# Kernel optimization log

Hardware: AMD Instinct MI355X
Metric: run time of the kernel (lower is better)

Reference implementation:

```python
import jax, jax.numpy as jnp
import numpy as np
import math

B, S, E, H = 2, 1024, 1024, 8
HD = E // H
M, W, K, GH, R, MR = 128, 32, 8, 128, 8, 8
ATTN_ALPHA, GATE_TEMP, CONTENT_MIX = 3.0, 1.0, 0.25
FFN_H = 4 * E


def _layernorm(z, g, b):
    mu = jnp.mean(z, axis=-1, keepdims=True)
    var = jnp.var(z, axis=-1, keepdims=True)
    return (z - mu) * jax.lax.rsqrt(var + 1e-5) * g + b


def _topk_sparse(logits, k, temp):
    # faithful to torch topk_sparse_weights: hard + (soft - hard).detach()
    soft = jax.nn.softmax(logits / max(temp, 1e-6), axis=-1)
    idx = jax.lax.top_k(soft, k)[1]
    hard = jax.nn.one_hot(idx, logits.shape[-1], dtype=soft.dtype).sum(axis=-2)
    hard = hard / (hard.sum(axis=-1, keepdims=True) + 1e-8)
    return hard + jax.lax.stop_gradient(soft - hard)


def _pos_and_window():
    rel = jnp.arange(-(S - 1), S, dtype=jnp.float32)  # [2S-1]
    p1 = rel / S
    p2 = jnp.sign(rel) * jnp.sqrt(jnp.abs(rel) + 1e-6) / math.sqrt(S)
    pos_kern = jnp.stack([p1, p2], axis=-1)  # [2S-1, 2]
    d = jnp.arange(S, dtype=jnp.float32)
    sigma = S / 4.0
    win = jnp.exp(-(d ** 2) / (2.0 * sigma ** 2))  # [S]
    return pos_kern, win


def setup_inputs() -> dict:
    key = jax.random.key(0)
    ks = jax.random.split(key, 20)
    rn = lambda i, shape, s: jax.random.normal(ks[i], shape, dtype=jnp.float32) * s
    scale = 1.0 / math.sqrt(HD)
    return {
        'x': rn(0, (B, S, E), 1.0),
        'v_w': rn(1, (E, E), 0.02), 'v_b': jnp.zeros((E,), jnp.float32),
        'out_w': rn(2, (E, E), 0.02), 'out_b': jnp.zeros((E,), jnp.float32),
        'qmod_w': rn(3, (E, H), 0.02), 'qmod_b': jnp.zeros((H,), jnp.float32),
        'kmod_w': rn(4, (E, H), 0.02), 'kmod_b': jnp.zeros((H,), jnp.float32),
        'gate_w1': rn(5, (H, E, GH), 0.02), 'gate_b1': jnp.zeros((H, GH), jnp.float32),
        'gate_w2': rn(6, (H, GH, M), 0.02), 'gate_b2': jnp.zeros((H, M), jnp.float32),
        'mod_w1': rn(7, (H, E, GH), 0.02), 'mod_b1': jnp.zeros((H, GH), jnp.float32),
        'mod_w2': rn(8, (H, GH, MR), 0.02), 'mod_b2': jnp.zeros((H, MR), jnp.float32),
        'mod_basis': rn(9, (H, MR, M), 0.05),
        'freqs': rn(10, (H, M, W, 2), 1.5),
        'amps': rn(11, (H, M, W), 0.02) + 0.5,
        'phases': rn(12, (H, M, W), math.pi),
        'content_wq': rn(13, (H, HD, R), scale),
        'content_wk': rn(14, (H, HD, R), scale),
        'ffn_w1': rn(15, (E, FFN_H), 0.02), 'ffn_b1': jnp.zeros((FFN_H,), jnp.float32),
        'ffn_w2': rn(16, (FFN_H, E), 0.02), 'ffn_b2': jnp.zeros((E,), jnp.float32),
        'ln_attn_g': jnp.ones((E,), jnp.float32), 'ln_attn_b': jnp.zeros((E,), jnp.float32),
        'ln_ffn_g': jnp.ones((E,), jnp.float32), 'ln_ffn_b': jnp.zeros((E,), jnp.float32),
    }


def reference(x, v_w, v_b, out_w, out_b, qmod_w, qmod_b, kmod_w, kmod_b,
              gate_w1, gate_b1, gate_w2, gate_b2, mod_w1, mod_b1, mod_w2, mod_b2,
              mod_basis, freqs, amps, phases, content_wq, content_wk,
              ffn_w1, ffn_b1, ffn_w2, ffn_b2, ln_attn_g, ln_attn_b, ln_ffn_g, ln_ffn_b):
    pos_kern, win = _pos_and_window()
    # --- per-sequence gating over mask library (top-k sparse routing) ---
    pooled = x.mean(axis=1)  # [B,E]
    gh = jax.nn.relu(jnp.einsum('be,heg->bhg', pooled, gate_w1) + gate_b1)
    glog = jnp.einsum('bhg,hgm->bhm', gh, gate_w2) + gate_b2  # [B,H,M]
    wsel = _topk_sparse(glog, K, GATE_TEMP)
    mh = jax.nn.relu(jnp.einsum('be,heg->bhg', pooled, mod_w1) + mod_b1)
    mr = jnp.einsum('bhg,hgr->bhr', mh, mod_w2) + mod_b2  # [B,H,MR]
    mod = jnp.einsum('bhr,hrm->bhm', mr, mod_basis)
    wmod = wsel * (1.0 + mod)  # [B,H,M]
    # --- wave-interference synthesis of relative-position kernels ---
    dots = jnp.einsum('ld,hmwd->hmwl', pos_kern, freqs)  # [H,M,W,2S-1]
    waves = jnp.sin(2.0 * math.pi * dots + phases[..., None]) * amps[..., None]
    kernels = waves.sum(axis=2)  # [H,M,2S-1]
    kern = jnp.einsum('bhm,hml->bhl', wmod, kernels)  # [B,H,2S-1]
    # --- Toeplitz gather into causal score matrix ---
    i = jnp.arange(S)
    rel_idx = (i[None, :] - i[:, None]) + (S - 1)  # index of rel = j - i
    scores = kern[:, :, rel_idx]  # [B,H,S,S]
    dist = jnp.clip(i[:, None] - i[None, :], 0, S - 1)
    scores = scores * win[dist]
    qs = x @ qmod_w + qmod_b  # [B,S,H]
    km = x @ kmod_w + kmod_b
    logits = ATTN_ALPHA * scores + qs.transpose(0, 2, 1)[..., None] + km.transpose(0, 2, 1)[:, :, None, :]
    # --- low-rank content term ---
    xh = x.reshape(B, S, H, HD)
    qc = jnp.einsum('bshd,hdr->bhsr', xh, content_wq)
    kc = jnp.einsum('bshd,hdr->bhsr', xh, content_wk)
    logits = logits + CONTENT_MIX * jnp.einsum('bhsr,bhtr->bhst', qc, kc)
    causal = i[:, None] >= i[None, :]
    logits = jnp.where(causal, logits, -jnp.inf)
    attn = jax.nn.softmax(logits, axis=-1)
    v = (x @ v_w + v_b).reshape(B, S, H, HD)
    o = jnp.einsum('bhst,bthd->bshd', attn, v).reshape(B, S, E)
    o = o @ out_w + out_b
    y = _layernorm(x + o, ln_attn_g, ln_attn_b)
    f = jax.nn.gelu(y @ ffn_w1 + ffn_b1) @ ffn_w2 + ffn_b2
    return _layernorm(y + f, ln_ffn_g, ln_ffn_b)
```

## Files before the change

kernel.cpp:

```cpp
#include <hip/hip_runtime.h>
#include <math.h>
#include <stdint.h>

namespace {

constexpr int B_ = 2, S_ = 1024, E_ = 1024, H_ = 8, HD_ = 128;
constexpr int M_ = 128, W_ = 32, GH_ = 128, R_ = 8, MR_ = 8, FFNH_ = 4096;
constexpr int SCH = 32;
constexpr int SPC = S_ / SCH;

typedef __bf16 bf16;
typedef _Float16 f16;
typedef __attribute__((ext_vector_type(8))) __bf16 bf16x8;
typedef __attribute__((ext_vector_type(4))) __bf16 bf16x4;
typedef __attribute__((ext_vector_type(4))) _Float16 f16x4;
typedef __attribute__((ext_vector_type(4))) float f32x4;

__device__ inline float gelu_tanh(float u) {
  float u3 = u * u * u;
  return 0.5f * u * (1.f + tanhf(0.7978845608028654f * (u + 0.044715f * u3)));
}

__device__ __forceinline__ void gl_lds16(const void* g, void* l) {
  __builtin_amdgcn_global_load_lds((const __attribute__((address_space(1))) void*)g,
                                   (__attribute__((address_space(3))) void*)l, 16, 0, 0);
}

__global__ __launch_bounds__(256) void k_prep(
    const float* __restrict__ x, bf16* __restrict__ xb,
    const float* __restrict__ v_w, bf16* __restrict__ vwT,
    const float* __restrict__ out_w, bf16* __restrict__ outwT,
    const float* __restrict__ ffn_w1, bf16* __restrict__ ffn1T,
    const float* __restrict__ ffn_w2, bf16* __restrict__ ffn2T,
    const float* __restrict__ qmw, const float* __restrict__ kmw,
    const float* __restrict__ cwq, const float* __restrict__ cwk,
    bf16* __restrict__ wcat, float* __restrict__ part,
    const float* __restrict__ freqs, const float* __restrict__ amps,
    const float* __restrict__ phases, float* __restrict__ kerns) {
  __shared__ float tile[32][33];
  __shared__ float f0[W_], f1[W_], am[W_], ph[W_];
  int b = blockIdx.x, t = threadIdx.x;
  if (b < 2048) {
    size_t i = ((size_t)b * 256 + t) * 4;
    float4 v = *(const float4*)(x + i);
    bf16x4 o;
    o.x = (bf16)v.x; o.y = (bf16)v.y; o.z = (bf16)v.z; o.w = (bf16)v.w;
    *(bf16x4*)(xb + i) = o;
    return;
  }
  if (b < 12288) {
    const float* w; bf16* wT; int K, N, bx, by;
    if (b < 3072) {
      w = v_w; wT = vwT; K = 1024; N = 1024;
      int l = b - 2048; bx = l & 31; by = l >> 5;
    } else if (b < 4096) {
      w = out_w; wT = outwT; K = 1024; N = 1024;
      int l = b - 3072; bx = l & 31; by = l >> 5;
    } else if (b < 8192) {
      w = ffn_w1; wT = ffn1T; K = 1024; N = 4096;
      int l = b - 4096; bx = l & 127; by = l >> 7;
    } else {
      w = ffn_w2; wT = ffn2T; K = 4096; N = 1024;
      int l = b - 8192; bx = l & 31; by = l >> 5;
    }
    int n0 = bx * 32, k0 = by * 32;
    int tx = t & 31, ty = t >> 5;
    for (int r = ty; r < 32; r += 8) tile[r][tx] = w[(size_t)(k0 + r) * N + n0 + tx];
    __syncthreads();
    for (int r = ty; r < 32; r += 8) wT[(size_t)(n0 + r) * K + k0 + tx] = (bf16)tile[tx][r];
    return;
  }
  if (b < 13312) {
    int idx = (b - 12288) * 256 + t;
    int n = idx >> 10, k = idx & 1023;
    float v = 0.f;
    if (n < 8) {
      v = qmw[k * 8 + n];
    } else if (n < 16) {
      v = kmw[k * 8 + (n - 8)];
    } else if (n < 80) {
      int u = n - 16, h = u >> 3, r = u & 7;
      int kk = k - h * 128;
      if (kk >= 0 && kk < 128) v = cwq[((size_t)h * 128 + kk) * 8 + r];
    } else if (n < 144) {
      int u = n - 80, h = u >> 3, r = u & 7;
      int kk = k - h * 128;
      if (kk >= 0 && kk < 128) v = cwk[((size_t)h * 128 + kk) * 8 + r];
    }
    wcat[idx] = (bf16)v;
    return;
  }
  if (b < 13376) {
    int b0 = b - 13312;
    int bb = b0 / SCH, c = b0 % SCH;
    const float* xp = x + (size_t)bb * S_ * E_ + (size_t)c * SPC * E_;
    float acc[4] = {0.f, 0.f, 0.f, 0.f};
    for (int s = 0; s < SPC; ++s) {
      const float* row = xp + (size_t)s * E_;
#pragma unroll
      for (int q = 0; q < 4; ++q) acc[q] += row[t + q * 256];
    }
    float* pp = part + (size_t)b0 * E_;
#pragma unroll
    for (int q = 0; q < 4; ++q) pp[t + q * 256] = acc[q];
    return;
  }
  {
    int blk = b - 13376;
    int lt = blk & 3;
    int hm = blk >> 2;
    if (t < W_) {
      f0[t] = freqs[((size_t)hm * W_ + t) * 2 + 0];
      f1[t] = freqs[((size_t)hm * W_ + t) * 2 + 1];
      am[t] = amps[(size_t)hm * W_ + t];
      ph[t] = phases[(size_t)hm * W_ + t];
    }
    __syncthreads();
    int l = lt * 256 + t;
    float rel = (float)(l - (S_ - 1));
    float p1 = rel * (1.0f / S_);
    float p2 = (rel < 0.f) ? (-sqrtf(-rel + 1e-6f) * (1.0f / 32.0f)) : 0.f;
    const float TWO_PI = 6.28318530717958647692f;
    float acc = 0.f;
#pragma unroll
    for (int w = 0; w < W_; ++w)
      acc += am[w] * __sinf(TWO_PI * (f0[w] * p1 + f1[w] * p2) + ph[w]);
    kerns[(size_t)hm * S_ + l] = acc;
  }
}

__global__ __launch_bounds__(256) void k_fin_qk(
    const f16* __restrict__ P, const float* __restrict__ qmb,
    const float* __restrict__ kmb, float* __restrict__ qsT,
    float* __restrict__ kmT, float* __restrict__ qc, float* __restrict__ kc) {
  int row = blockIdx.x;
  int t = threadIdx.x;
  if (t >= 144) return;
  int b = row >> 10, s = row & 1023;
  const size_t mn = (size_t)2048 * 256;
  float sum = 0.f;
#pragma unroll
  for (int z = 0; z < 8; ++z) sum += (float)P[(size_t)z * mn + (size_t)row * 256 + t];
  if (t < 8) {
    qsT[((size_t)(b * 8 + t)) * 1024 + s] = sum + qmb[t];
  } else if (t < 16) {
    kmT[((size_t)(b * 8 + t - 8)) * 1024 + s] = sum + kmb[t - 8];
  } else if (t < 80) {
    int u = t - 16, h = u >> 3, r = u & 7;
    qc[(((size_t)(b * 8 + h)) * 1024 + s) * 8 + r] = sum;
  } else {
    int u = t - 80, h = u >> 3, r = u & 7;
    kc[(((size_t)(b * 8 + h)) * 1024 + s) * 8 + r] = sum;
  }
}

__global__ __launch_bounds__(256) void k_gate1(
    const float* __restrict__ part,
    const float* __restrict__ gw1, const float* __restrict__ mw1,
    float2* __restrict__ outp) {
  int chunk = blockIdx.x;
  int h = blockIdx.y;
  int mat = blockIdx.z;
  const float* w = mat ? mw1 : gw1;
  int t = threadIdx.x;
  __shared__ float spool[2][64];
  if (t < 128) {
    int bb = t >> 6;
    int e = chunk * 64 + (t & 63);
    float s = 0.f;
    for (int c = 0; c < SCH; ++c) s += part[(size_t)(bb * SCH + c) * E_ + e];
    spool[bb][t & 63] = s * (1.0f / S_);
  }
  __syncthreads();
  int g = t & 127, half = t >> 7;
  int e0 = chunk * 64 + half * 32;
  const float* wp = w + (size_t)h * E_ * GH_ + (size_t)e0 * GH_ + g;
  float a0 = 0.f, a1 = 0.f;
#pragma unroll 8
  for (int r = 0; r < 32; ++r) {
    float wv = wp[(size_t)r * GH_];
    a0 += spool[0][half * 32 + r] * wv;
    a1 += spool[1][half * 32 + r] * wv;
  }
  __shared__ float red[2][2][128];
  red[half][0][g] = a0;
  red[half][1][g] = a1;
  __syncthreads();
  if (half == 0) {
    float2 o;
    o.x = red[0][0][g] + red[1][0][g];
    o.y = red[0][1][g] + red[1][1][g];
    outp[(((size_t)mat * H_ + h) * 16 + chunk) * 128 + g] = o;
  }
}

__global__ __launch_bounds__(256) void k_gate2(
    const float2* __restrict__ part,
    const float* __restrict__ gb1, const float* __restrict__ gw2, const float* __restrict__ gb2,
    const float* __restrict__ mb1, const float* __restrict__ mw2, const float* __restrict__ mb2,
    const float* __restrict__ mbasis, float* __restrict__ wmod) {
  int bh = blockIdx.x;
  int b = bh >> 3, h = bh & 7;
  int t = threadIdx.x;
  __shared__ float ghs[GH_], mhs[GH_], glog[M_], mrs[MR_];
  __shared__ float red2[2][128];
  __shared__ float rbuf[128];
  {
    int g = t & 127, mat = t >> 7;
    const float2* pp = part + ((size_t)mat * H_ + h) * 16 * 128 + g;
    float acc = 0.f;
#pragma unroll
    for (int c = 0; c < 16; ++c) {
      float2 v = pp[(size_t)c * 128];
      acc += b ? v.y : v.x;
    }
    acc += (mat ? mb1 : gb1)[h * GH_ + g];
    acc = fmaxf(acc, 0.f);
    if (mat == 0) ghs[g] = acc; else mhs[g] = acc;
  }
  __syncthreads();
  {
    int m = t & 127, half = t >> 7;
    float acc = 0.f;
    const float* wp = gw2 + (size_t)h * GH_ * M_ + m;
#pragma unroll 4
    for (int g = half * 64; g < half * 64 + 64; ++g)
      acc += ghs[g] * wp[(size_t)g * M_];
    red2[half][m] = acc;
  }
  __syncthreads();
  if (t < 128) glog[t] = red2[0][t] + red2[1][t] + gb2[h * M_ + t];
  if (t < 64) {
    int r = t & 7, seg = t >> 3;
    float acc = 0.f;
    const float* wp = mw2 + (size_t)h * GH_ * MR_ + r;
    for (int g = seg * 16; g < seg * 16 + 16; ++g) acc += mhs[g] * wp[(size_t)g * MR_];
    acc += __shfl_xor(acc, 8);
    acc += __shfl_xor(acc, 16);
    acc += __shfl_xor(acc, 32);
    if (t < 8) mrs[t] = acc + mb2[h * MR_ + t];
  }
  __syncthreads();
  if (t < 128) rbuf[t] = glog[t];
  __syncthreads();
  for (int off = 64; off >= 1; off >>= 1) {
    if (t < off) rbuf[t] = fmaxf(rbuf[t], rbuf[t + off]);
    __syncthreads();
  }
  float mx = rbuf[0];
  __syncthreads();
  float ev = 0.f;
  if (t < 128) ev = expf(glog[t] - mx);
  __syncthreads();
  if (t < 128) rbuf[t] = ev;
  __syncthreads();
  for (int off = 64; off >= 1; off >>= 1) {
    if (t < off) rbuf[t] += rbuf[t + off];
    __syncthreads();
  }
  float inv = 1.f / rbuf[0];
  if (t < 128) {
    float wsel = ev * inv;
    float md = 0.f;
#pragma unroll
    for (int r = 0; r < MR_; ++r) md += mrs[r] * mbasis[((size_t)h * MR_ + r) * M_ + t];
    wmod[bh * M_ + t] = wsel * (1.f + md);
  }
}

__global__ __launch_bounds__(256) void k_cont(const float* __restrict__ qc,
                                              const float* __restrict__ kc,
                                              bf16* __restrict__ cont,
                                              const float* __restrict__ wmod,
                                              const float* __restrict__ kerns,
                                              float* __restrict__ swin) {
  int jt = blockIdx.x, it = blockIdx.y;
  int bh = blockIdx.z;
  int t = threadIdx.x;
  if (bh == 16) {
    __shared__ float wm[M_];
    int blk = it * 8 + jt;
    int dt = blk & 3;
    int sbh = blk >> 2;
    int h = sbh & 7;
    if (t < M_) wm[t] = wmod[sbh * M_ + t];
    __syncthreads();
    int d = dt * 256 + t;
    int l = (S_ - 1) - d;
    float acc = 0.f;
    for (int m = 0; m < M_; ++m) acc += wm[m] * kerns[((size_t)h * M_ + m) * S_ + l];
    float dd = (float)d;
    float win = expf(-dd * dd * (1.0f / 131072.0f));
    swin[(size_t)sbh * S_ + d] = 3.0f * win * acc;
    return;
  }
  if (jt > it) return;
  int w = t >> 6, lane = t & 63;
  int ln = lane & 15, ko = lane >> 4;
  int i0 = it * 128 + w * 32;
  int j0 = jt * 128;

  bf16x8 av[2];
#pragma unroll
  for (int mi = 0; mi < 2; ++mi) {
    bf16x8 a;
#pragma unroll
    for (int k = 0; k < 8; ++k) a[k] = (bf16)0.f;
    if (ko == 0) {
      const float* qp = &qc[((size_t)bh * S_ + i0 + mi * 16 + ln) * 8];
      float4 q0 = *(const float4*)qp;
      float4 q1 = *(const float4*)(qp + 4);
      a[0] = (bf16)q0.x; a[1] = (bf16)q0.y; a[2] = (bf16)q0.z; a[3] = (bf16)q0.w;
      a[4] = (bf16)q1.x; a[5] = (bf16)q1.y; a[6] = (bf16)q1.z; a[7] = (bf16)q1.w;
    }
    av[mi] = a;
  }
  bf16x8 bv[8];
#pragma unroll
  for (int nb = 0; nb < 8; ++nb) {
    bf16x8 bb;
#pragma unroll
    for (int k = 0; k < 8; ++k) bb[k] = (bf16)0.f;
    if (ko == 0) {
      const float* kp = &kc[((size_t)bh * S_ + j0 + nb * 16 + ln) * 8];
      float4 k0 = *(const float4*)kp;
      float4 k1 = *(const float4*)(kp + 4);
      bb[0] = (bf16)k0.x; bb[1] = (bf16)k0.y; bb[2] = (bf16)k0.z; bb[3] = (bf16)k0.w;
      bb[4] = (bf16)k1.x; bb[5] = (bf16)k1.y; bb[6] = (bf16)k1.z; bb[7] = (bf16)k1.w;
    }
    bv[nb] = bb;
  }
  f32x4 acc[2][8];
#pragma unroll
  for (int mi = 0; mi < 2; ++mi)
#pragma unroll
    for (int nb = 0; nb < 8; ++nb) {
      acc[mi][nb] = (f32x4){0.f, 0.f, 0.f, 0.f};
      acc[mi][nb] = __builtin_amdgcn_mfma_f32_16x16x32_bf16(av[mi], bv[nb], acc[mi][nb], 0, 0, 0);
    }
  bf16* cb = cont + ((size_t)bh << 20);
#pragma unroll
  for (int mi = 0; mi < 2; ++mi)
#pragma unroll
    for (int nb = 0; nb < 8; ++nb) {
      int col = j0 + nb * 16 + ln;
#pragma unroll
      for (int reg = 0; reg < 4; ++reg) {
        int row = i0 + mi * 16 + ko * 4 + reg;
        cb[(size_t)row * S_ + col] = (bf16)acc[mi][nb][reg];
      }
    }
}

template <bool GELU, bool RES, bool OUTF32, bool OUTBF16>
__global__ __launch_bounds__(256) void k_gemm_mfma(
    const bf16* __restrict__ A, const bf16* __restrict__ BT,
    const float* __restrict__ bias, const float* __restrict__ res,
    float* __restrict__ C, bf16* __restrict__ Cb, int N, int K) {
  __shared__ bf16 Asb[2][8192];
  __shared__ bf16 Bsb[2][8192];
  int t = threadIdx.x;
  int gx = gridDim.x, gy = gridDim.y;
  int nwg = gx * gy;
  int lin = blockIdx.y * gx + blockIdx.x;
  if (!(nwg & 7)) {
    int cpx = nwg >> 3;
    lin = (lin & 7) * cpx + (lin >> 3);
  }
  int by = lin % gy;
  int bx = lin / gy;
  int row0 = by * 128, col0 = bx * 128;
  int lane = t & 63, wid = t >> 6;
  int wr = wid >> 1, wc = wid & 1;

  const bf16* AgP[4];
  const bf16* BgP[4];
  int ldo[4];
#pragma unroll
  for (int j = 0; j < 4; ++j) {
    int p = t + j * 256;
    int sub = p >> 9;
    int pp = p & 511;
    int rt = ((pp >> 6) << 4) | (pp & 15);
    int kb = (pp >> 4) & 3;
    AgP[j] = A + (size_t)(row0 + rt) * K + sub * 32 + kb * 8;
    BgP[j] = BT + (size_t)(col0 + rt) * K + sub * 32 + kb * 8;
    ldo[j] = sub * 4096 + pp * 8;
  }

  f32x4 acc[4][4];
#pragma unroll
  for (int m = 0; m < 4; ++m)
#pragma unroll
    for (int n = 0; n < 4; ++n) acc[m][n] = (f32x4){0.f, 0.f, 0.f, 0.f};

#pragma unroll
  for (int j = 0; j < 4; ++j) {
    gl_lds16(AgP[j], &Asb[0][ldo[j]]);
    gl_lds16(BgP[j], &Bsb[0][ldo[j]]);
  }

  const int nt = K >> 6;
  for (int kt = 0; kt < nt; ++kt) {
    int cur = kt & 1;
    __syncthreads();
    if (kt + 1 < nt) {
      size_t go = (size_t)(kt + 1) * 64;
      int nb = cur ^ 1;
#pragma unroll
      for (int j = 0; j < 4; ++j) {
        gl_lds16(AgP[j] + go, &Asb[nb][ldo[j]]);
        gl_lds16(BgP[j] + go, &Bsb[nb][ldo[j]]);
      }
    }
#pragma unroll
    for (int kk = 0; kk < 2; ++kk) {
      bf16x8 af[4], bfr[4];
#pragma unroll
      for (int m = 0; m < 4; ++m)
        af[m] = *(const bf16x8*)&Asb[cur][kk * 4096 + ((wr * 4 + m) * 64 + lane) * 8];
#pragma unroll
      for (int n = 0; n < 4; ++n)
        bfr[n] = *(const bf16x8*)&Bsb[cur][kk * 4096 + ((wc * 4 + n) * 64 + lane) * 8];
#pragma unroll
      for (int m = 0; m < 4; ++m)
#pragma unroll
        for (int n = 0; n < 4; ++n)
          acc[m][n] = __builtin_amdgcn_mfma_f32_16x16x32_bf16(af[m], bfr[n], acc[m][n], 0, 0, 0);
    }
  }

  int r0 = row0 + wr * 64, c0 = col0 + wc * 64;
#pragma unroll
  for (int m = 0; m < 4; ++m) {
#pragma unroll
    for (int n = 0; n < 4; ++n) {
      int col = c0 + n * 16 + (lane & 15);
      float bcol = bias[col];
#pragma unroll
      for (int reg = 0; reg < 4; ++reg) {
        int row = r0 + m * 16 + ((lane >> 4) << 2) + reg;
        float u = acc[m][n][reg] + bcol;
        if (GELU) u = gelu_tanh(u);
        if (RES) u += res[(size_t)row * N + col];
        if (OUTF32) C[(size_t)row * N + col] = u;
        if (OUTBF16) Cb[(size_t)row * N + col] = (bf16)u;
      }
    }
  }
}

template <int NB>
__global__ __launch_bounds__(256) void k_gemm_sk(
    const bf16* __restrict__ A, const bf16* __restrict__ BT,
    f16* __restrict__ P, int N, int K, int Kslice, size_t strideB, size_t mn) {
  __shared__ bf16 Asb[2][8192];
  __shared__ bf16 Bsb[2][8192];
  int t = threadIdx.x;
  int gx = gridDim.x, gy = gridDim.y;
  int nwg = gx * gy * gridDim.z;
  int lin = (blockIdx.z * gy + blockIdx.y) * gx + blockIdx.x;
  if (!(nwg & 7)) {
    int cpx = nwg >> 3;
    lin = (lin & 7) * cpx + (lin >> 3);
  }
  int by = lin % gy;
  int rem = lin / gy;
  int bx = rem % gx;
  int z = rem / gx;

  int bb = z % NB;
  int k0 = (z / NB) * Kslice;
  const bf16* Bbase = BT + (size_t)bb * strideB;
  int row0 = by * 128, col0 = bx * 128;
  int lane = t & 63, wid = t >> 6;
  int wr = wid >> 1, wc = wid & 1;

  const bf16* AgP[4];
  const bf16* BgP[4];
  int ldo[4];
#pragma unroll
  for (int j = 0; j < 4; ++j) {
    int p = t + j * 256;
    int sub = p >> 9;
    int pp = p & 511;
    int rt = ((pp >> 6) << 4) | (pp & 15);
    int kb = (pp >> 4) & 3;
    AgP[j] = A + (size_t)(row0 + rt) * K + k0 + sub * 32 + kb * 8;
    BgP[j] = Bbase + (size_t)(col0 + rt) * K + k0 + sub * 32 + kb * 8;
    ldo[j] = sub * 4096 + pp * 8;
  }

  f32x4 acc[4][4];
#pragma unroll
  for (int m = 0; m < 4; ++m)
#pragma unroll
    for (int n = 0; n < 4; ++n) acc[m][n] = (f32x4){0.f, 0.f, 0.f, 0.f};

#pragma unroll
  for (int j = 0; j < 4; ++j) {
    gl_lds16(AgP[j], &Asb[0][ldo[j]]);
    gl_lds16(BgP[j], &Bsb[0][ldo[j]]);
  }

  const int nt = Kslice >> 6;
  for (int kt = 0; kt < nt; ++kt) {
    int cur = kt & 1;
    __syncthreads();
    if (kt + 1 < nt) {
      size_t go = (size_t)(kt + 1) * 64;
      int nb = cur ^ 1;
#pragma unroll
      for (int j = 0; j < 4; ++j) {
        gl_lds16(AgP[j] + go, &Asb[nb][ldo[j]]);
        gl_lds16(BgP[j] + go, &Bsb[nb][ldo[j]]);
      }
    }
#pragma unroll
    for (int kk = 0; kk < 2; ++kk) {
      bf16x8 af[4], bfr[4];
#pragma unroll
      for (int m = 0; m < 4; ++m)
        af[m] = *(const bf16x8*)&Asb[cur][kk * 4096 + ((wr * 4 + m) * 64 + lane) * 8];
#pragma unroll
      for (int n = 0; n < 4; ++n)
        bfr[n] = *(const bf16x8*)&Bsb[cur][kk * 4096 + ((wc * 4 + n) * 64 + lane) * 8];
#pragma unroll
      for (int m = 0; m < 4; ++m)
#pragma unroll
        for (int n = 0; n < 4; ++n)
          acc[m][n] = __builtin_amdgcn_mfma_f32_16x16x32_bf16(af[m], bfr[n], acc[m][n], 0, 0, 0);
    }
  }

  f16* Pz = P + (size_t)z * mn;
  int r0 = row0 + wr * 64, c0 = col0 + wc * 64;
#pragma unroll
  for (int m = 0; m < 4; ++m)
#pragma unroll
    for (int n = 0; n < 4; ++n) {
      int col = c0 + n * 16 + (lane & 15);
#pragma unroll
      for (int reg = 0; reg < 4; ++reg) {
        int row = r0 + m * 16 + ((lane >> 4) << 2) + reg;
        Pz[(size_t)row * N + col] = (f16)acc[m][n][reg];
      }
    }
}

__global__ __launch_bounds__(256) void k_fin_vT(const f16* __restrict__ P,
                                                const float* __restrict__ bias,
                                                bf16* __restrict__ vT) {
  size_t i = ((size_t)blockIdx.x * 256 + threadIdx.x) * 4;
  const size_t mn = (size_t)1024 * 1024;
  float sx = 0.f, sy = 0.f, sz = 0.f, sw2 = 0.f;
#pragma unroll
  for (int sk = 0; sk < 4; ++sk) {
    f16x4 v = *(const f16x4*)&P[(size_t)sk * 2 * mn + i];
    sx += (float)v.x; sy += (float)v.y; sz += (float)v.z; sw2 += (float)v.w;
  }
  float bcol = bias[(i >> 10) & 1023];
  bf16x4 o;
  o.x = (bf16)(sx + bcol); o.y = (bf16)(sy + bcol);
  o.z = (bf16)(sz + bcol); o.w = (bf16)(sw2 + bcol);
  *(bf16x4*)&vT[i] = o;
}

template <int SK, bool OUTBF16>
__global__ __launch_bounds__(256) void k_fin_ln(
    const f16* __restrict__ P, const float* __restrict__ bias,
    const float* __restrict__ res, const float* __restrict__ g,
    const float* __restrict__ bb, float* __restrict__ outF,
    bf16* __restrict__ outB) {
  int row = blockIdx.x, t = threadIdx.x;
  size_t base = (size_t)row * E_ + t * 4;
  const size_t mn = (size_t)2048 * 1024;
  float u0 = 0.f, u1 = 0.f, u2 = 0.f, u3 = 0.f;
#pragma unroll
  for (int sk = 0; sk < SK; ++sk) {
    f16x4 v = *(const f16x4*)&P[(size_t)sk * mn + base];
    u0 += (float)v.x; u1 += (float)v.y; u2 += (float)v.z; u3 += (float)v.w;
  }
  float4 bv = *(const float4*)&bias[t * 4];
  float4 rv = *(const float4*)&res[base];
  u0 += bv.x + rv.x; u1 += bv.y + rv.y; u2 += bv.z + rv.z; u3 += bv.w + rv.w;
  float s = u0 + u1 + u2 + u3;
  float s2 = u0 * u0 + u1 * u1 + u2 * u2 + u3 * u3;
#pragma unroll
  for (int off = 32; off >= 1; off >>= 1) {
    s += __shfl_xor(s, off);
    s2 += __shfl_xor(s2, off);
  }
  __shared__ float rs[4], rs2[4];
  int wid = t >> 6;
  if ((t & 63) == 0) { rs[wid] = s; rs2[wid] = s2; }
  __syncthreads();
  float S1 = rs[0] + rs[1] + rs[2] + rs[3];
  float S2 = rs2[0] + rs2[1] + rs2[2] + rs2[3];
  float mu = S1 * (1.f / E_);
  float var = S2 * (1.f / E_) - mu * mu;
  float inv = rsqrtf(var + 1e-5f);
  float4 gv = *(const float4*)&g[t * 4];
  float4 bbv = *(const float4*)&bb[t * 4];
  float4 ov;
  ov.x = (u0 - mu) * inv * gv.x + bbv.x;
  ov.y = (u1 - mu) * inv * gv.y + bbv.y;
  ov.z = (u2 - mu) * inv * gv.z + bbv.z;
  ov.w = (u3 - mu) * inv * gv.w + bbv.w;
  *(float4*)&outF[base] = ov;
  if (OUTBF16) {
    bf16x4 obv;
    obv.x = (bf16)ov.x; obv.y = (bf16)ov.y; obv.z = (bf16)ov.z; obv.w = (bf16)ov.w;
    *(bf16x4*)&outB[base] = obv;
  }
}

__global__ __launch_bounds__(256) void k_attn2(
    const float* __restrict__ qsT, const float* __restrict__ kmT,
    const bf16* __restrict__ cont, const float* __restrict__ swin,
    const bf16* __restrict__ vT,
    bf16* __restrict__ o, bf16* __restrict__ opart, float* __restrict__ mlpart) {
  int q = blockIdx.x & 3;
  int iwg = blockIdx.x >> 2;
  if (q > iwg) return;
  int bh = blockIdx.y;
  int b = bh >> 3, h = bh & 7;
  int t = threadIdx.x;
  int wid = t >> 6, lane = t & 63;
  int iw = iwg * 4 + wid;
  int m = lane & 15, ko = lane >> 4;
  int ntile = iwg + 1;

  __shared__ float sw[S_];
  *(float4*)&sw[t * 4] = *(const float4*)&swin[(size_t)bh * S_ + t * 4];
  __syncthreads();

  int i_row = iw * 16 + m;
  float qs_i = qsT[(size_t)bh * S_ + i_row];
  const bf16* cr = cont + ((size_t)bh << 20) + (size_t)i_row * S_;

  f32x4 acc[8];
#pragma unroll
  for (int nf = 0; nf < 8; ++nf) acc[nf] = (f32x4){0.f, 0.f, 0.f, 0.f};
  float m_run = -INFINITY, l_run = 0.f;

  for (int jt = q; jt < ntile; jt += 4) {
    int j0 = jt * 64;
    float pv[2][8];
    float mx = -INFINITY;
    bf16x8 cv[2];
    cv[0] = *(const bf16x8*)&cr[j0 + ko * 8];
    cv[1] = *(const bf16x8*)&cr[j0 + 32 + ko * 8];
#pragma unroll
    for (int s = 0; s < 2; ++s) {
      int bj = j0 + s * 32 + ko * 8;
      float4 km0 = *(const float4*)&kmT[(size_t)bh * S_ + bj];
      float4 km1 = *(const float4*)&kmT[(size_t)bh * S_ + bj + 4];
      float kmv[8] = {km0.x, km0.y, km0.z, km0.w, km1.x, km1.y, km1.z, km1.w};
#pragma unroll
      for (int e = 0; e < 8; ++e) {
        int j = bj + e;
        int dd = i_row - j;
        float val = sw[dd >= 0 ? dd : 0] + qs_i + kmv[e] + 0.25f * (float)cv[s][e];
        val = (dd >= 0) ? val : -INFINITY;
        pv[s][e] = val;
        mx = fmaxf(mx, val);
      }
    }
    mx = fmaxf(mx, __shfl_xor(mx, 16));
    mx = fmaxf(mx, __shfl_xor(mx, 32));
    float mnew = fmaxf(m_run, mx);
    float scale = __expf(m_run - mnew);
    float lsum = 0.f;
    bf16x8 pa[2];
#pragma unroll
    for (int s = 0; s < 2; ++s)
#pragma unroll
      for (int e = 0; e < 8; ++e) {
        float p = __expf(pv[s][e] - mnew);
        lsum += p;
        pa[s][e] = (bf16)p;
      }
    lsum += __shfl_xor(lsum, 16);
    lsum += __shfl_xor(lsum, 32);
    l_run = l_run * scale + lsum;
    m_run = mnew;
    float sc[4];
#pragma unroll
    for (int r = 0; r < 4; ++r) sc[r] = __shfl(scale, ko * 4 + r);
#pragma unroll
    for (int nf = 0; nf < 8; ++nf)
#pragma unroll
      for (int r = 0; r < 4; ++r) acc[nf][r] *= sc[r];
#pragma unroll
    for (int s = 0; s < 2; ++s) {
      int bj = j0 + s * 32 + ko * 8;
#pragma unroll
      for (int nf = 0; nf < 8; ++nf) {
        int d = nf * 16 + m;
        bf16x8 bv = *(const bf16x8*)&vT[((size_t)bh * HD_ + d) * S_ + bj];
        acc[nf] = __builtin_amdgcn_mfma_f32_16x16x32_bf16(pa[s], bv, acc[nf], 0, 0, 0);
      }
    }
  }

  if (ntile == 1) {
    float lr[4];
#pragma unroll
    for (int r = 0; r < 4; ++r) lr[r] = __shfl(l_run, ko * 4 + r);
#pragma unroll
    for (int nf = 0; nf < 8; ++nf) {
      int d = nf * 16 + m;
#pragma unroll
      for (int r = 0; r < 4; ++r) {
        int row = iw * 16 + ko * 4 + r;
        o[(((size_t)b * S_ + row) * H_ + h) * HD_ + d] = (bf16)(acc[nf][r] / lr[r]);
      }
    }
  } else {
    bf16* op = opart + ((size_t)(q * 16 + bh) * 64 + iw) * 2048;
#pragma unroll
    for (int nf = 0; nf < 8; ++nf) {
      int d = nf * 16 + m;
#pragma unroll
      for (int r = 0; r < 4; ++r) op[(ko * 4 + r) * 128 + d] = (bf16)acc[nf][r];
    }
    if (lane < 16) {
      float* mlp = mlpart + ((size_t)(q * 16 + bh) * 64 + iw) * 32;
      mlp[m * 2 + 0] = m_run;
      mlp[m * 2 + 1] = l_run;
    }
  }
}

__global__ __launch_bounds__(256) void k_comb(const bf16* __restrict__ opart,
                                              const float* __restrict__ mlpart,
                                              bf16* __restrict__ o) {
  int blk = blockIdx.x;
  int bh = blk / 60, iw = blk % 60 + 4;
  int b = bh >> 3, h = bh & 7;
  int t = threadIdx.x;
  int r = t >> 4, d0 = (t & 15) * 8;
  int nq = iw / 4 + 1;
  if (nq > 4) nq = 4;
  float mq[4], lq[4];
  float mm = -INFINITY;
#pragma unroll
  for (int q = 0; q < 4; ++q) {
    if (q < nq) {
      size_t idx = (size_t)(q * 16 + bh) * 64 + iw;
      mq[q] = mlpart[idx * 32 + r * 2];
      lq[q] = mlpart[idx * 32 + r * 2 + 1];
      mm = fmaxf(mm, mq[q]);
    }
  }
  float L = 0.f;
  float acc[8] = {0.f, 0.f, 0.f, 0.f, 0.f, 0.f, 0.f, 0.f};
#pragma unroll
  for (int q = 0; q < 4; ++q) {
    if (q < nq) {
      float e = __expf(mq[q] - mm);
      L += lq[q] * e;
      size_t idx = (size_t)(q * 16 + bh) * 64 + iw;
      bf16x8 v = *(const bf16x8*)&opart[(idx * 16 + r) * 128 + d0];
#pragma unroll
      for (int k = 0; k < 8; ++k) acc[k] += (float)v[k] * e;
    }
  }
  float inv = 1.f / L;
  bf16x8 ov;
#pragma unroll
  for (int k = 0; k < 8; ++k) ov[k] = (bf16)(acc[k] * inv);
  int row = iw * 16 + r;
  *(bf16x8*)&o[(((size_t)b * S_ + row) * H_ + h) * HD_ + d0] = ov;
}

}

extern "C" void kernel_launch(void* const* d_in, const int* in_sizes, int n_in,
                              void* d_out, int out_size, void* d_ws, size_t ws_size,
                              hipStream_t stream) {
  (void)in_sizes; (void)n_in; (void)out_size; (void)ws_size;
  const float* x       = (const float*)d_in[0];
  const float* v_w     = (const float*)d_in[1];
  const float* v_b     = (const float*)d_in[2];
  const float* out_w   = (const float*)d_in[3];
  const float* out_b   = (const float*)d_in[4];
  const float* qmod_w  = (const float*)d_in[5];
  const float* qmod_b  = (const float*)d_in[6];
  const float* kmod_w  = (const float*)d_in[7];
  const float* kmod_b  = (const float*)d_in[8];
  const float* gate_w1 = (const float*)d_in[9];
  const float* gate_b1 = (const float*)d_in[10];
  const float* gate_w2 = (const float*)d_in[11];
  const float* gate_b2 = (const float*)d_in[12];
  const float* mod_w1  = (const float*)d_in[13];
  const float* mod_b1  = (const float*)d_in[14];
  const float* mod_w2  = (const float*)d_in[15];
  const float* mod_b2  = (const float*)d_in[16];
  const float* mod_basis = (const float*)d_in[17];
  const float* freqs   = (const float*)d_in[18];
  const float* amps    = (const float*)d_in[19];
  const float* phases  = (const float*)d_in[20];
  const float* cwq     = (const float*)d_in[21];
  const float* cwk     = (const float*)d_in[22];
  const float* ffn_w1  = (const float*)d_in[23];
  const float* ffn_b1  = (const float*)d_in[24];
  const float* ffn_w2  = (const float*)d_in[25];
  const float* ffn_b2  = (const float*)d_in[26];
  const float* ln_ag   = (const float*)d_in[27];
  const float* ln_ab   = (const float*)d_in[28];
  const float* ln_fg   = (const float*)d_in[29];
  const float* ln_fb   = (const float*)d_in[30];

  char* wsc = (char*)d_ws;
  size_t off = 0;
  auto alloc = [&](size_t bytes) -> void* {
    void* p = wsc + off;
    off += (bytes + 255) & ~(size_t)255;
    return p;
  };
  float* pooled = (float*)alloc(2048 * 4);
  float* part   = (float*)alloc(65536 * 4);
  float2* gpart = (float2*)alloc((size_t)2 * H_ * 16 * 128 * 8);
  float* wmod   = (float*)alloc(2048 * 4);
  float* kerns  = (float*)alloc((size_t)H_ * M_ * S_ * 4);
  float* swin   = (float*)alloc((size_t)B_ * H_ * S_ * 4);
  float* qsT    = (float*)alloc((size_t)B_ * H_ * S_ * 4);
  float* kmT    = (float*)alloc((size_t)B_ * H_ * S_ * 4);
  float* qcb    = (float*)alloc((size_t)B_ * H_ * S_ * R_ * 4);
  float* kcb    = (float*)alloc((size_t)B_ * H_ * S_ * R_ * 4);
  float* ybuf   = (float*)alloc((size_t)B_ * S_ * E_ * 4);
  bf16* xb      = (bf16*)alloc((size_t)B_ * S_ * E_ * 2);
  bf16* yb      = (bf16*)alloc((size_t)B_ * S_ * E_ * 2);
  bf16* vwT     = (bf16*)alloc((size_t)E_ * E_ * 2);
  bf16* outwT   = (bf16*)alloc((size_t)E_ * E_ * 2);
  bf16* ffn1T   = (bf16*)alloc((size_t)E_ * FFNH_ * 2);
  bf16* ffn2T   = (bf16*)alloc((size_t)FFNH_ * E_ * 2);
  bf16* wcatT   = (bf16*)alloc((size_t)256 * E_ * 2);
  bf16* vT      = (bf16*)alloc((size_t)B_ * S_ * E_ * 2);
  bf16* ob      = (bf16*)alloc((size_t)B_ * S_ * E_ * 2);
  float* mlpart = (float*)alloc((size_t)4 * 16 * 64 * 16 * 2 * 4);
  char* poolU2  = (char*)alloc((size_t)B_ * S_ * FFNH_ * 2);
  bf16* opart = (bf16*)poolU2;
  bf16* hb    = (bf16*)poolU2;
  char* P1c = (char*)alloc((size_t)64 * 1024 * 1024);
  f16*  P1  = (f16*)P1c;
  bf16* cont = (bf16*)(P1c + (size_t)16 * 1024 * 1024);
  (void)pooled;

  float* outp = (float*)d_out;
  const int BS = B_ * S_;

  k_prep<<<17472, 256, 0, stream>>>(x, xb, v_w, vwT, out_w, outwT,
                                    ffn_w1, ffn1T, ffn_w2, ffn2T,
                                    qmod_w, kmod_w, cwq, cwk, wcatT,
                                    part, freqs, amps, phases, kerns);

  k_gate1<<<dim3(16, H_, 2), 256, 0, stream>>>(part, gate_w1, mod_w1, gpart);
  k_gate2<<<B_ * H_, 256, 0, stream>>>(gpart, gate_b1, gate_w2, gate_b2,
                                       mod_b1, mod_w2, mod_b2, mod_basis, wmod);

  k_gemm_sk<1><<<dim3(2, 16, 8), 256, 0, stream>>>(
      xb, wcatT, P1, 256, E_, 128, 0, (size_t)2048 * 256);
  k_fin_qk<<<2048, 256, 0, stream>>>(P1, qmod_b, kmod_b, qsT, kmT, qcb, kcb);

  k_cont<<<dim3(8, 8, 17), 256, 0, stream>>>(qcb, kcb, cont, wmod, kerns, swin);

  k_gemm_sk<2><<<dim3(8, 8, 8), 256, 0, stream>>>(
      vwT, xb, P1, S_, E_, 256, (size_t)S_ * E_, (size_t)1024 * 1024);
  k_fin_vT<<<2048, 256, 0, stream>>>(P1, v_b, vT);

  k_attn2<<<dim3(64, 16), 256, 0, stream>>>(qsT, kmT, cont, swin, vT, ob, opart, mlpart);
  k_comb<<<16 * 60, 256, 0, stream>>>(opart, mlpart, ob);

  k_gemm_sk<1><<<dim3(8, 16, 4), 256, 0, stream>>>(
      ob, outwT, P1, E_, E_, 256, 0, (size_t)2048 * 1024);
  k_fin_ln<4, true><<<2048, 256, 0, stream>>>(P1, out_b, x, ln_ag, ln_ab, ybuf, yb);

  k_gemm_mfma<true, false, false, true><<<dim3(FFNH_ / 128, BS / 128), 256, 0, stream>>>(
      yb, ffn1T, ffn_b1, nullptr, nullptr, hb, FFNH_, E_);

  k_gemm_sk<1><<<dim3(8, 16, 4), 256, 0, stream>>>(
      hb, ffn2T, P1, E_, FFNH_, 1024, 0, (size_t)2048 * 1024);
  k_fin_ln<4, false><<<2048, 256, 0, stream>>>(P1, ffn_b2, ybuf, ln_fg, ln_fb, outp, nullptr);
}
```

Baseline: 236.5 us.

## Merge independent pre-attention kernels into shared launches by block-index partitioning

The GEMM mainloop moves into a reusable device function. Three pairs of independent kernels now share one launch each, with the work picked by block index: the q/k projection GEMM with the first gate layer, the q/k finalization with the second gate layer, and the content/window kernel with the value projection GEMM. This cuts the number of kernel launches and the gaps between them, and lets unrelated small workloads run alongside the GEMMs. In exchange, every block in a merged launch reserves the GEMM's larger LDS footprint, which can lower occupancy for the lightweight branches.

```diff
diff --git a/kernel.cpp b/kernel.cpp
--- a/kernel.cpp
+++ b/kernel.cpp
@@ -24,6 +24,95 @@
 __device__ __forceinline__ void gl_lds16(const void* g, void* l) {
   __builtin_amdgcn_global_load_lds((const __attribute__((address_space(1))) void*)g,
                                    (__attribute__((address_space(3))) void*)l, 16, 0, 0);
+}
+
+template <int NB>
+__device__ __forceinline__ void gemm_body(
+    const bf16* __restrict__ A, const bf16* __restrict__ BT,
+    f16* __restrict__ P, int N, int K, int Kslice, size_t strideB, size_t mn,
+    int lin, int gx, int gy, bf16* Asb, bf16* Bsb) {
+  int t = threadIdx.x;
+  int by = lin % gy;
+  int rem = lin / gy;
+  int bx = rem % gx;
+  int z = rem / gx;
+  int bb = z % NB;
+  int k0 = (z / NB) * Kslice;
+  const bf16* Bbase = BT + (size_t)bb * strideB;
+  int row0 = by * 128, col0 = bx * 128;
+  int lane = t & 63, wid = t >> 6;
+  int wr = wid >> 1, wc = wid & 1;
+
+  const bf16* AgP[4];
+  const bf16* BgP[4];
+  int ldo[4];
+#pragma unroll
+  for (int j = 0; j < 4; ++j) {
+    int p = t + j * 256;
+    int sub = p >> 9;
+    int pp = p & 511;
+    int rt = ((pp >> 6) << 4) | (pp & 15);
+    int kb = (pp >> 4) & 3;
+    AgP[j] = A + (size_t)(row0 + rt) * K + k0 + sub * 32 + kb * 8;
+    BgP[j] = Bbase + (size_t)(col0 + rt) * K + k0 + sub * 32 + kb * 8;
+    ldo[j] = sub * 4096 + pp * 8;
+  }
+
+  f32x4 acc[4][4];
+#pragma unroll
+  for (int m = 0; m < 4; ++m)
+#pragma unroll
+    for (int n = 0; n < 4; ++n) acc[m][n] = (f32x4){0.f, 0.f, 0.f, 0.f};
+
+#pragma unroll
+  for (int j = 0; j < 4; ++j) {
+    gl_lds16(AgP[j], &Asb[ldo[j]]);
+    gl_lds16(BgP[j], &Bsb[ldo[j]]);
+  }
+
+  const int nt = Kslice >> 6;
+  for (int kt = 0; kt < nt; ++kt) {
+    int cur = kt & 1;
+    __syncthreads();
+    if (kt + 1 < nt) {
+      size_t go = (size_t)(kt + 1) * 64;
+      int nb = cur ^ 1;
+#pragma unroll
+      for (int j = 0; j < 4; ++j) {
+        gl_lds16(AgP[j] + go, &Asb[nb * 8192 + ldo[j]]);
+        gl_lds16(BgP[j] + go, &Bsb[nb * 8192 + ldo[j]]);
+      }
+    }
+#pragma unroll
+    for (int kk = 0; kk < 2; ++kk) {
+      bf16x8 af[4], bfr[4];
+#pragma unroll
+      for (int m = 0; m < 4; ++m)
+        af[m] = *(const bf16x8*)&Asb[cur * 8192 + kk * 4096 + ((wr * 4 + m) * 64 + lane) * 8];
+#pragma unroll
+      for (int n = 0; n < 4; ++n)
+        bfr[n] = *(const bf16x8*)&Bsb[cur * 8192 + kk * 4096 + ((wc * 4 + n) * 64 + lane) * 8];
+#pragma unroll
+      for (int m = 0; m < 4; ++m)
+#pragma unroll
+        for (int n = 0; n < 4; ++n)
+          acc[m][n] = __builtin_amdgcn_mfma_f32_16x16x32_bf16(af[m], bfr[n], acc[m][n], 0, 0, 0);
+    }
+  }
+
+  f16* Pz = P + (size_t)z * mn;
+  int r0 = row0 + wr * 64, c0 = col0 + wc * 64;
+#pragma unroll
+  for (int m = 0; m < 4; ++m)
+#pragma unroll
+    for (int n = 0; n < 4; ++n) {
+      int col = c0 + n * 16 + (lane & 15);
+#pragma unroll
+      for (int reg = 0; reg < 4; ++reg) {
+        int row = r0 + m * 16 + ((lane >> 4) << 2) + reg;
+        Pz[(size_t)row * N + col] = (f16)acc[m][n][reg];
+      }
+    }
 }
 
 __global__ __launch_bounds__(256) void k_prep(
@@ -129,41 +218,26 @@
   }
 }
 
-__global__ __launch_bounds__(256) void k_fin_qk(
-    const f16* __restrict__ P, const float* __restrict__ qmb,
-    const float* __restrict__ kmb, float* __restrict__ qsT,
-    float* __restrict__ kmT, float* __restrict__ qc, float* __restrict__ kc) {
-  int row = blockIdx.x;
-  int t = threadIdx.x;
-  if (t >= 144) return;
-  int b = row >> 10, s = row & 1023;
-  const size_t mn = (size_t)2048 * 256;
-  float sum = 0.f;
-#pragma unroll
-  for (int z = 0; z < 8; ++z) sum += (float)P[(size_t)z * mn + (size_t)row * 256 + t];
-  if (t < 8) {
-    qsT[((size_t)(b * 8 + t)) * 1024 + s] = sum + qmb[t];
-  } else if (t < 16) {
-    kmT[((size_t)(b * 8 + t - 8)) * 1024 + s] = sum + kmb[t - 8];
-  } else if (t < 80) {
-    int u = t - 16, h = u >> 3, r = u & 7;
-    qc[(((size_t)(b * 8 + h)) * 1024 + s) * 8 + r] = sum;
-  } else {
-    int u = t - 80, h = u >> 3, r = u & 7;
-    kc[(((size_t)(b * 8 + h)) * 1024 + s) * 8 + r] = sum;
-  }
-}
-
-__global__ __launch_bounds__(256) void k_gate1(
+__global__ __launch_bounds__(256) void k_qkg(
+    const bf16* __restrict__ xb, const bf16* __restrict__ wcatT,
+    f16* __restrict__ P,
     const float* __restrict__ part,
     const float* __restrict__ gw1, const float* __restrict__ mw1,
-    float2* __restrict__ outp) {
-  int chunk = blockIdx.x;
-  int h = blockIdx.y;
-  int mat = blockIdx.z;
+    float2* __restrict__ gpart) {
+  __shared__ bf16 Asb[2 * 8192];
+  __shared__ bf16 Bsb[2 * 8192];
+  __shared__ float spool[2][64];
+  __shared__ float red[2][2][128];
+  int b = blockIdx.x, t = threadIdx.x;
+  if (b < 256) {
+    int lin = (b & 7) * 32 + (b >> 3);
+    gemm_body<1>(xb, wcatT, P, 256, E_, 128, 0, (size_t)2048 * 256,
+                 lin, 2, 16, Asb, Bsb);
+    return;
+  }
+  int b0 = b - 256;
+  int chunk = b0 & 15, h = (b0 >> 4) & 7, mat = b0 >> 7;
   const float* w = mat ? mw1 : gw1;
-  int t = threadIdx.x;
-  __shared__ float spool[2][64];
   if (t < 128) {
     int bb = t >> 6;
     int e = chunk * 64 + (t & 63);
@@ -182,7 +256,6 @@
     a0 += spool[0][half * 32 + r] * wv;
     a1 += spool[1][half * 32 + r] * wv;
   }
-  __shared__ float red[2][2][128];
   red[half][0][g] = a0;
   red[half][1][g] = a1;
   __syncthreads();
@@ -190,24 +263,48 @@
     float2 o;
     o.x = red[0][0][g] + red[1][0][g];
     o.y = red[0][1][g] + red[1][1][g];
-    outp[(((size_t)mat * H_ + h) * 16 + chunk) * 128 + g] = o;
-  }
-}
-
-__global__ __launch_bounds__(256) void k_gate2(
-    const float2* __restrict__ part,
+    gpart[(((size_t)mat * H_ + h) * 16 + chunk) * 128 + g] = o;
+  }
+}
+
+__global__ __launch_bounds__(256) void k_fg2(
+    const f16* __restrict__ P, const float* __restrict__ qmb,
+    const float* __restrict__ kmb, float* __restrict__ qsT,
+    float* __restrict__ kmT, float* __restrict__ qc, float* __restrict__ kc,
+    const float2* __restrict__ gpart,
     const float* __restrict__ gb1, const float* __restrict__ gw2, const float* __restrict__ gb2,
     const float* __restrict__ mb1, const float* __restrict__ mw2, const float* __restrict__ mb2,
     const float* __restrict__ mbasis, float* __restrict__ wmod) {
-  int bh = blockIdx.x;
-  int b = bh >> 3, h = bh & 7;
-  int t = threadIdx.x;
   __shared__ float ghs[GH_], mhs[GH_], glog[M_], mrs[MR_];
   __shared__ float red2[2][128];
   __shared__ float rbuf[128];
+  int blk = blockIdx.x, t = threadIdx.x;
+  if (blk < 2048) {
+    if (t >= 144) return;
+    int row = blk;
+    int b = row >> 10, s = row & 1023;
+    const size_t mn = (size_t)2048 * 256;
+    float sum = 0.f;
+#pragma unroll
+    for (int z = 0; z < 8; ++z) sum += (float)P[(size_t)z * mn + (size_t)row * 256 + t];
+    if (t < 8) {
+      qsT[((size_t)(b * 8 + t)) * 1024 + s] = sum + qmb[t];
+    } else if (t < 16) {
+      kmT[((size_t)(b * 8 + t - 8)) * 1024 + s] = sum + kmb[t - 8];
+    } else if (t < 80) {
+      int u = t - 16, h = u >> 3, r = u & 7;
+      qc[(((size_t)(b * 8 + h)) * 1024 + s) * 8 + r] = sum;
+    } else {
+      int u = t - 80, h = u >> 3, r = u & 7;
+      kc[(((size_t)(b * 8 + h)) * 1024 + s) * 8 + r] = sum;
+    }
+    return;
+  }
+  int bh = blk - 2048;
+  int b = bh >> 3, h = bh & 7;
   {
     int g = t & 127, mat = t >> 7;
-    const float2* pp = part + ((size_t)mat * H_ + h) * 16 * 128 + g;
+    const float2* pp = gpart + ((size_t)mat * H_ + h) * 16 * 128 + g;
     float acc = 0.f;
 #pragma unroll
     for (int c = 0; c < 16; ++c) {
@@ -268,17 +365,26 @@
   }
 }
 
-__global__ __launch_bounds__(256) void k_cont(const float* __restrict__ qc,
-                                              const float* __restrict__ kc,
-                                              bf16* __restrict__ cont,
-                                              const float* __restrict__ wmod,
-                                              const float* __restrict__ kerns,
-                                              float* __restrict__ swin) {
-  int jt = blockIdx.x, it = blockIdx.y;
-  int bh = blockIdx.z;
-  int t = threadIdx.x;
+__global__ __launch_bounds__(256) void k_cv(
+    const float* __restrict__ qc, const float* __restrict__ kc,
+    bf16* __restrict__ cont,
+    const float* __restrict__ wmod, const float* __restrict__ kerns,
+    float* __restrict__ swin,
+    const bf16* __restrict__ vwT, const bf16* __restrict__ xb,
+    f16* __restrict__ P) {
+  __shared__ bf16 Asb[2 * 8192];
+  __shared__ bf16 Bsb[2 * 8192];
+  __shared__ float wm[M_];
+  int b = blockIdx.x, t = threadIdx.x;
+  if (b >= 1088) {
+    int l = b - 1088;
+    int lin = (l & 7) * 64 + (l >> 3);
+    gemm_body<2>(vwT, xb, P, S_, E_, 256, (size_t)S_ * E_, (size_t)1024 * 1024,
+                 lin, 8, 8, Asb, Bsb);
+    return;
+  }
+  int jt = b & 7, it = (b >> 3) & 7, bh = b >> 6;
   if (bh == 16) {
-    __shared__ float wm[M_];
     int blk = it * 8 + jt;
     int dt = blk & 3;
     int sbh = blk >> 2;
@@ -454,9 +560,8 @@
 __global__ __launch_bounds__(256) void k_gemm_sk(
     const bf16* __restrict__ A, const bf16* __restrict__ BT,
     f16* __restrict__ P, int N, int K, int Kslice, size_t strideB, size_t mn) {
-  __shared__ bf16 Asb[2][8192];
-  __shared__ bf16 Bsb[2][8192];
-  int t = threadIdx.x;
+  __shared__ bf16 Asb[2 * 8192];
+  __shared__ bf16 Bsb[2 * 8192];
   int gx = gridDim.x, gy = gridDim.y;
   int nwg = gx * gy * gridDim.z;
   int lin = (blockIdx.z * gy + blockIdx.y) * gx + blockIdx.x;
@@ -464,88 +569,7 @@
     int cpx = nwg >> 3;
     lin = (lin & 7) * cpx + (lin >> 3);
   }
-  int by = lin % gy;
-  int rem = lin / gy;
-  int bx = rem % gx;
-  int z = rem / gx;
-
-  int bb = z % NB;
-  int k0 = (z / NB) * Kslice;
-  const bf16* Bbase = BT + (size_t)bb * strideB;
-  int row0 = by * 128, col0 = bx * 128;
-  int lane = t & 63, wid = t >> 6;
-  int wr = wid >> 1, wc = wid & 1;
-
-  const bf16* AgP[4];
-  const bf16* BgP[4];
-  int ldo[4];
-#pragma unroll
-  for (int j = 0; j < 4; ++j) {
-    int p = t + j * 256;
-    int sub = p >> 9;
-    int pp = p & 511;
-    int rt = ((pp >> 6) << 4) | (pp & 15);
-    int kb = (pp >> 4) & 3;
-    AgP[j] = A + (size_t)(row0 + rt) * K + k0 + sub * 32 + kb * 8;
-    BgP[j] = Bbase + (size_t)(col0 + rt) * K + k0 + sub * 32 + kb * 8;
-    ldo[j] = sub * 4096 + pp * 8;
-  }
-
-  f32x4 acc[4][4];
-#pragma unroll
-  for (int m = 0; m < 4; ++m)
-#pragma unroll
-    for (int n = 0; n < 4; ++n) acc[m][n] = (f32x4){0.f, 0.f, 0.f, 0.f};
-
-#pragma unroll
-  for (int j = 0; j < 4; ++j) {
-    gl_lds16(AgP[j], &Asb[0][ldo[j]]);
-    gl_lds16(BgP[j], &Bsb[0][ldo[j]]);
-  }
-
-  const int nt = Kslice >> 6;
-  for (int kt = 0; kt < nt; ++kt) {
-    int cur = kt & 1;
-    __syncthreads();
-    if (kt + 1 < nt) {
-      size_t go = (size_t)(kt + 1) * 64;
-      int nb = cur ^ 1;
-#pragma unroll
-      for (int j = 0; j < 4; ++j) {
-        gl_lds16(AgP[j] + go, &Asb[nb][ldo[j]]);
-        gl_lds16(BgP[j] + go, &Bsb[nb][ldo[j]]);
-      }
-    }
-#pragma unroll
-    for (int kk = 0; kk < 2; ++kk) {
-      bf16x8 af[4], bfr[4];
-#pragma unroll
-      for (int m = 0; m < 4; ++m)
-        af[m] = *(const bf16x8*)&Asb[cur][kk * 4096 + ((wr * 4 + m) * 64 + lane) * 8];
-#pragma unroll
-      for (int n = 0; n < 4; ++n)
-        bfr[n] = *(const bf16x8*)&Bsb[cur][kk * 4096 + ((wc * 4 + n) * 64 + lane) * 8];
-#pragma unroll
-      for (int m = 0; m < 4; ++m)
-#pragma unroll
-        for (int n = 0; n < 4; ++n)
-          acc[m][n] = __builtin_amdgcn_mfma_f32_16x16x32_bf16(af[m], bfr[n], acc[m][n], 0, 0, 0);
-    }
-  }
-
-  f16* Pz = P + (size_t)z * mn;
-  int r0 = row0 + wr * 64, c0 = col0 + wc * 64;
-#pragma unroll
-  for (int m = 0; m < 4; ++m)
-#pragma unroll
-    for (int n = 0; n < 4; ++n) {
-      int col = c0 + n * 16 + (lane & 15);
-#pragma unroll
-      for (int reg = 0; reg < 4; ++reg) {
-        int row = r0 + m * 16 + ((lane >> 4) << 2) + reg;
-        Pz[(size_t)row * N + col] = (f16)acc[m][n][reg];
-      }
-    }
+  gemm_body<NB>(A, BT, P, N, K, Kslice, strideB, mn, lin, gx, gy, Asb, Bsb);
 }
 
 __global__ __launch_bounds__(256) void k_fin_vT(const f16* __restrict__ P,
@@ -857,18 +881,14 @@
                                     qmod_w, kmod_w, cwq, cwk, wcatT,
                                     part, freqs, amps, phases, kerns);
 
-  k_gate1<<<dim3(16, H_, 2), 256, 0, stream>>>(part, gate_w1, mod_w1, gpart);
-  k_gate2<<<B_ * H_, 256, 0, stream>>>(gpart, gate_b1, gate_w2, gate_b2,
-                                       mod_b1, mod_w2, mod_b2, mod_basis, wmod);
-
-  k_gemm_sk<1><<<dim3(2, 16, 8), 256, 0, stream>>>(
-      xb, wcatT, P1, 256, E_, 128, 0, (size_t)2048 * 256);
-  k_fin_qk<<<2048, 256, 0, stream>>>(P1, qmod_b, kmod_b, qsT, kmT, qcb, kcb);
-
-  k_cont<<<dim3(8, 8, 17), 256, 0, stream>>>(qcb, kcb, cont, wmod, kerns, swin);
-
-  k_gemm_sk<2><<<dim3(8, 8, 8), 256, 0, stream>>>(
-      vwT, xb, P1, S_, E_, 256, (size_t)S_ * E_, (size_t)1024 * 1024);
+  k_qkg<<<512, 256, 0, stream>>>(xb, wcatT, P1, part, gate_w1, mod_w1, gpart);
+
+  k_fg2<<<2064, 256, 0, stream>>>(P1, qmod_b, kmod_b, qsT, kmT, qcb, kcb,
+                                  gpart, gate_b1, gate_w2, gate_b2,
+                                  mod_b1, mod_w2, mod_b2, mod_basis, wmod);
+
+  k_cv<<<1600, 256, 0, stream>>>(qcb, kcb, cont, wmod, kerns, swin,
+                                 vwT, xb, P1);
   k_fin_vT<<<2048, 256, 0, stream>>>(P1, v_b, vT);
 
   k_attn2<<<dim3(64, 16), 256, 0, stream>>>(qsT, kmT, cont, swin, vT, ob, opart, mlpart);
```

After: 228.2 us. 1.04x faster.
